# Kernel tuning notes

Hardware: AMD Instinct MI355X
Metric: run time of the kernel (lower is better)

Reference implementation:

```python
import jax, jax.numpy as jnp
import numpy as np

K_SIZE = 7
D_MODEL = 128
D_Q = 64
N_HEADS = 4
D_FF = 512
EPS = 1e-5


def _windows(x, k):
    # x: [N,E,H,W] -> [N,E,P,H,W]; zero-padded local k x k windows,
    # row-major over (dy,dx), matching nn.Unfold ordering.
    p = k // 2
    N, E, H, W = x.shape
    xp = jnp.pad(x, ((0, 0), (0, 0), (p, p), (p, p)))
    ws = [xp[:, :, i:i + H, j:j + W] for i in range(k) for j in range(k)]
    return jnp.stack(ws, axis=2)


def _layernorm(x, g, b):
    m = jnp.mean(x, -1, keepdims=True)
    v = jnp.var(x, -1, keepdims=True)
    return (x - m) * jax.lax.rsqrt(v + EPS) * g + b


def setup_inputs() -> dict:
    key = jax.random.key(0)
    ks = jax.random.split(key, 12)
    E, Q, F = D_MODEL, D_Q, D_FF

    def g(k, shape, s=0.02):
        return jax.random.normal(k, shape, jnp.float32) * s

    return dict(
        x=jax.random.normal(ks[0], (4, E, 64, 64), jnp.float32),
        qcoeff=jax.random.normal(ks[1], (4, Q), jnp.float32),
        wq=g(ks[2], (E, E)), bq=jnp.zeros((E,), jnp.float32),
        wk=g(ks[3], (E, E)), bk=jnp.zeros((E,), jnp.float32),
        wv=g(ks[4], (E, E)), bv=jnp.zeros((E,), jnp.float32),
        rel_bias=jnp.zeros((N_HEADS, K_SIZE * K_SIZE), jnp.float32),
        ln1_g=jnp.ones((E,), jnp.float32), ln1_b=jnp.zeros((E,), jnp.float32),
        bil_w=g(ks[5], (E, E, Q)), bil_b=jnp.zeros((E,), jnp.float32),
        ln2_g=jnp.ones((E,), jnp.float32), ln2_b=jnp.zeros((E,), jnp.float32),
        w1=g(ks[6], (F, E)), b1=jnp.zeros((F,), jnp.float32),
        w2=g(ks[7], (E, F)), b2=jnp.zeros((E,), jnp.float32),
    )


def reference(x, qcoeff, wq, bq, wk, bk, wv, bv, rel_bias, ln1_g, ln1_b,
              bil_w, bil_b, ln2_g, ln2_b, w1, b1, w2, b2):
    N, E, H, W = x.shape
    Nh = N_HEADS
    Hd = E // Nh
    P = K_SIZE * K_SIZE

    x_nhwc = jnp.transpose(x, (0, 2, 3, 1))              # [N,H,W,E]
    xn = _layernorm(x_nhwc, ln1_g, ln1_b)
    xnc = jnp.transpose(xn, (0, 3, 1, 2))                # [N,E,H,W]

    # 1x1-conv projections
    q = jnp.einsum('nchw,oc->nohw', xnc, wq) + bq[None, :, None, None]
    k = jnp.einsum('nchw,oc->nohw', xnc, wk) + bk[None, :, None, None]
    v = jnp.einsum('nchw,oc->nohw', xnc, wv) + bv[None, :, None, None]

    # local windows of K/V: [N,Nh,Hd,P,H,W]
    Kw = _windows(k, K_SIZE).reshape(N, Nh, Hd, P, H, W)
    Vw = _windows(v, K_SIZE).reshape(N, Nh, Hd, P, H, W)
    Qh = q.reshape(N, Nh, Hd, H, W)

    scores = jnp.einsum('nhdyx,nhdpyx->nhpyx', Qh, Kw)
    scores = scores + rel_bias[None, :, :, None, None]
    attn = jax.nn.softmax(scores, axis=2)                # softmax over P
    out = jnp.einsum('nhpyx,nhdpyx->nhdyx', attn, Vw).reshape(N, E, H, W)
    z0 = jnp.transpose(out, (0, 2, 3, 1))                # [N,H,W,E]

    # Bilinear(z0, qcoeff): qcoeff constant per (H,W) -> contract once per batch
    t = jnp.einsum('oiq,nq->noi', bil_w, qcoeff)         # [N,E,E]
    z1 = jnp.einsum('nhwi,noi->nhwo', z0, t) + bil_b

    z2 = z1 + x_nhwc
    z3 = _layernorm(z2, ln2_g, ln2_b)
    h1 = jax.nn.gelu(z3 @ w1.T + b1, approximate=False)  # dropout inactive (eval)
    z4 = h1 @ w2.T + b2 + z2
    return jnp.transpose(z4, (0, 3, 1, 2))               # [N,E,H,W]
```

## Files before the change

### kernel.cpp

```cpp
#include <hip/hip_runtime.h>
#include <cmath>

#define EPS 1e-5f
#define SZ 2097152

typedef __attribute__((ext_vector_type(8))) short short8;
typedef __attribute__((ext_vector_type(4))) float floatx4;

__device__ __forceinline__ float dot4(float4 a, float4 b) {
  return fmaf(a.x, b.x, fmaf(a.y, b.y, fmaf(a.z, b.z, a.w * b.w)));
}

__device__ __forceinline__ short f2bf(float f) {
  union { float f; unsigned u; } v; v.f = f;
  unsigned r = v.u + 0x7fff + ((v.u >> 16) & 1);
  return (short)(r >> 16);
}

#define MFMA16(a, b, c) __builtin_amdgcn_mfma_f32_16x16x32_bf16(a, b, c, 0, 0, 0)

__global__ __launch_bounds__(256) void k_prep(const float* __restrict__ w1,
    const float* __restrict__ w2, const float* __restrict__ wq,
    const float* __restrict__ wk, const float* __restrict__ wv,
    const float* __restrict__ bil_w, const float* __restrict__ qcoeff,
    short* __restrict__ w1bf, short* __restrict__ w2bf,
    short* __restrict__ wqbf, short* __restrict__ wkbf, short* __restrict__ wvbf,
    short* __restrict__ tb) {
  __shared__ float qs[256];
  int tid = threadIdx.x;
  qs[tid] = qcoeff[tid];
  __syncthreads();
  int tid0 = blockIdx.x * 256 + tid;
  int stride = gridDim.x * 256;
  for (int i = tid0; i < 16384; i += stride) {
    int flat = i * 4; int f = flat >> 7, c = flat & 127;
    float4 v = *(const float4*)&w1[flat];
    short t4[4] = {f2bf(v.x), f2bf(v.y), f2bf(v.z), f2bf(v.w)};
    *(uint2*)&w1bf[f * 136 + c] = *(uint2*)t4;
  }
  for (int i = tid0; i < 16384; i += stride) {
    int flat = i * 4; int o = flat >> 9, j = flat & 511;
    int ck = j >> 7, jj = j & 127;
    float4 v = *(const float4*)&w2[flat];
    short t4[4] = {f2bf(v.x), f2bf(v.y), f2bf(v.z), f2bf(v.w)};
    *(uint2*)&w2bf[(ck * 128 + o) * 136 + jj] = *(uint2*)t4;
  }
  for (int i = tid0; i < 4096; i += stride) {
    int flat = i * 4; int o = flat >> 7, c = flat & 127;
    float4 a = *(const float4*)&wq[flat];
    float4 b = *(const float4*)&wk[flat];
    float4 cc = *(const float4*)&wv[flat];
    short ta[4] = {f2bf(a.x), f2bf(a.y), f2bf(a.z), f2bf(a.w)};
    short tb4[4] = {f2bf(b.x), f2bf(b.y), f2bf(b.z), f2bf(b.w)};
    short tc[4] = {f2bf(cc.x), f2bf(cc.y), f2bf(cc.z), f2bf(cc.w)};
    *(uint2*)&wqbf[o * 136 + c] = *(uint2*)ta;
    *(uint2*)&wkbf[o * 136 + c] = *(uint2*)tb4;
    *(uint2*)&wvbf[o * 136 + c] = *(uint2*)tc;
  }
  {
    int flat = tid0;
    const float* wrow = bil_w + (size_t)flat * 64;
    float acc[4] = {0.f, 0.f, 0.f, 0.f};
    for (int qq = 0; qq < 64; qq += 4) {
      float4 w4 = *(const float4*)&wrow[qq];
#pragma unroll
      for (int nn = 0; nn < 4; ++nn) {
        const float* qc = &qs[nn * 64 + qq];
        acc[nn] = fmaf(w4.x, qc[0], fmaf(w4.y, qc[1], fmaf(w4.z, qc[2], fmaf(w4.w, qc[3], acc[nn]))));
      }
    }
    int o = flat >> 7, i = flat & 127;
#pragma unroll
    for (int nn = 0; nn < 4; ++nn) tb[nn * 17408 + o * 136 + i] = f2bf(acc[nn]);
  }
}

__global__ __launch_bounds__(1024) void k_qkvln(const float* __restrict__ x,
    const float* __restrict__ g, const float* __restrict__ b,
    const short* __restrict__ wqbf, const short* __restrict__ wkbf,
    const short* __restrict__ wvbf, const float* __restrict__ bq,
    const float* __restrict__ bk, const float* __restrict__ bv,
    float* __restrict__ xnhwc, short* __restrict__ qbf,
    short* __restrict__ kbf, short* __restrict__ vtb) {
  __shared__ float tile[128 * 65];
  __shared__ float mres[64], rres[64];
  __shared__ __align__(16) short xs[64 * 136];
  __shared__ __align__(16) short ws[128 * 136];
  int tid = threadIdx.x;
  int bid = blockIdx.x;
  int n = bid >> 6, y = bid & 63;
  const float* xb = x + (size_t)n * (128 * 4096) + y * 64;
  for (int it = 0; it < 8; ++it) {
    int flat = it * 1024 + tid;
    int c = flat >> 6, xp = flat & 63;
    tile[c * 65 + xp] = xb[(size_t)c * 4096 + xp];
  }
  __syncthreads();
  {
    int px = tid >> 4, cl = tid & 15;
    float s = 0.f, sq = 0.f;
#pragma unroll
    for (int j = 0; j < 8; ++j) {
      float v = tile[(cl * 8 + j) * 65 + px];
      s += v; sq += v * v;
    }
    s += __shfl_xor(s, 1);  sq += __shfl_xor(sq, 1);
    s += __shfl_xor(s, 2);  sq += __shfl_xor(sq, 2);
    s += __shfl_xor(s, 4);  sq += __shfl_xor(sq, 4);
    s += __shfl_xor(s, 8);  sq += __shfl_xor(sq, 8);
    if (cl == 0) {
      float m = s * (1.f / 128.f);
      float var = sq * (1.f / 128.f) - m * m;
      mres[px] = m;
      rres[px] = rsqrtf(var + EPS);
    }
  }
  __syncthreads();
  size_t rowbase = (size_t)bid * 8192;
  for (int it = 0; it < 8; ++it) {
    int flat = it * 1024 + tid;
    int c = flat & 127, px = flat >> 7;
    float v = tile[c * 65 + px];
    xnhwc[rowbase + flat] = v;
    xs[px * 136 + c] = f2bf((v - mres[px]) * rres[px] * g[c] + b[c]);
  }
  __syncthreads();
  int w = tid >> 6, lane = tid & 63;
  int quad = lane >> 4, r16 = lane & 15;
  int wm = w & 3, wn = w >> 2;
  int strip = wm * 16;
  short8 a[4];
#pragma unroll
  for (int kk = 0; kk < 4; ++kk)
    a[kk] = *(const short8*)&xs[(strip + r16) * 136 + kk * 32 + quad * 8];
  const short* wptr[3] = {wqbf, wkbf, wvbf};
  const float* bptr[3] = {bq, bk, bv};
  for (int m = 0; m < 3; ++m) {
    __syncthreads();
    const short* wp = wptr[m];
    for (int i = tid; i < 2176; i += 1024)
      *(short8*)&ws[i * 8] = *(const short8*)&wp[i * 8];
    __syncthreads();
    const float* bb = bptr[m];
#pragma unroll
    for (int nt = 0; nt < 2; ++nt) {
      int o0 = wn * 32 + nt * 16;
      floatx4 acc = {0.f, 0.f, 0.f, 0.f};
#pragma unroll
      for (int kk = 0; kk < 4; ++kk) {
        short8 bfr = *(const short8*)&ws[(o0 + r16) * 136 + kk * 32 + quad * 8];
        acc = MFMA16(a[kk], bfr, acc);
      }
      float bv2 = bb[o0 + r16];
      if (m < 2) {
        short* dst = (m == 0) ? qbf : kbf;
#pragma unroll
        for (int r = 0; r < 4; ++r) {
          int px = strip + quad * 4 + r;
          dst[rowbase + px * 128 + o0 + r16] = f2bf(acc[r] + bv2);
        }
      } else {
        short t4[4] = {f2bf(acc[0] + bv2), f2bf(acc[1] + bv2),
                       f2bf(acc[2] + bv2), f2bf(acc[3] + bv2)};
        *(uint2*)&vtb[(size_t)(n * 128 + o0 + r16) * 4096 + y * 64 + strip + quad * 4] =
            *(uint2*)t4;
      }
    }
  }
}

__global__ __launch_bounds__(256) void k_attn(const short* __restrict__ qbf,
    const short* __restrict__ kbf, const short* __restrict__ vtb,
    const float* __restrict__ rel_bias, float* __restrict__ z0) {
  __shared__ float ssf[4][16 * 50];
  __shared__ __align__(16) short AbB[4][16 * 68];
  __shared__ float biasS[4][52];
  int bid = blockIdx.x;
  int h = bid & 3, y = (bid >> 2) & 63, n = bid >> 8;
  int tid = threadIdx.x;
  int w = tid >> 6, lane = tid & 63;
  int quad = lane >> 4, r16 = lane & 15;
  int strip = w * 16;
  float* ssfw = ssf[w];
  short* Abw = AbB[w];
  float* biasw = biasS[w];
  {
    unsigned* ad = (unsigned*)Abw;
    for (int i = lane; i < 544; i += 64) ad[i] = 0u;
  }
  if (lane < 49) biasw[lane] = rel_bias[h * 49 + lane];
  const short* qrow = qbf + (size_t)n * 524288 + (size_t)y * 64 * 128 + h * 32;
  short8 qf = *(const short8*)&qrow[(strip + r16) * 128 + quad * 8];
  const short* kbp = kbf + (size_t)n * 524288 + h * 32;
#pragma unroll
  for (int r = 0; r < 7; ++r) {
    int yy = y + r - 3;
    bool yok = (unsigned)yy < 64u;
    int yyc = min(max(yy, 0), 63);
#pragma unroll
    for (int t = 0; t < 2; ++t) {
      int xxc = (w + t) * 16 + r16;
      int gx = xxc - 3;
      bool ok = yok && ((unsigned)gx < 64u);
      int gxc = min(max(gx, 0), 63);
      short8 bf = *(const short8*)&kbp[(size_t)(yyc * 64 + gxc) * 128 + quad * 8];
      floatx4 c = MFMA16(qf, bf, ((floatx4){0.f, 0.f, 0.f, 0.f}));
#pragma unroll
      for (int rr = 0; rr < 4; ++rr) {
        int lrow = quad * 4 + rr;
        int dx = xxc - (strip + lrow);
        if ((unsigned)dx < 7u) {
          float val = ok ? c[rr] : 0.f;
          ssfw[lrow * 50 + r * 7 + dx] = val + biasw[r * 7 + dx];
        }
      }
    }
  }
  {
    int lrow = lane >> 2, sub = lane & 3;
    int p0 = sub * 12, cnt = (sub == 3) ? 13 : 12;
    float sv[13];
    float mx = -1e30f;
    for (int pi = 0; pi < cnt; ++pi) { sv[pi] = ssfw[lrow * 50 + p0 + pi]; mx = fmaxf(mx, sv[pi]); }
    mx = fmaxf(mx, __shfl_xor(mx, 1));
    mx = fmaxf(mx, __shfl_xor(mx, 2));
    float sum = 0.f;
    for (int pi = 0; pi < cnt; ++pi) { float e = __expf(sv[pi] - mx); sv[pi] = e; sum += e; }
    sum += __shfl_xor(sum, 1);
    sum += __shfl_xor(sum, 2);
    float inv = 1.f / sum;
    for (int pi = 0; pi < cnt; ++pi) ssfw[lrow * 50 + p0 + pi] = sv[pi] * inv;
  }
  floatx4 oacc[2] = {(floatx4){0.f, 0.f, 0.f, 0.f}, (floatx4){0.f, 0.f, 0.f, 0.f}};
  int kk0 = (w == 3) ? 1 : 0;
  int kk1 = (w == 0) ? 0 : 1;
  int lrow = lane >> 2, sub = lane & 3;
  int pxg = strip + lrow;
  const short* vbp = vtb + (size_t)(n * 128 + h * 32) * 4096;
  for (int r = 0; r < 7; ++r) {
    int yy = y + r - 3;
    bool yok = (unsigned)yy < 64u;
    int yyc = min(max(yy, 0), 63);
    int c0 = pxg + sub - 3;
    if ((unsigned)c0 < 64u) Abw[lrow * 68 + c0] = f2bf(ssfw[lrow * 50 + r * 7 + sub]);
    int c1 = pxg + sub + 1;
    if (sub < 3 && (unsigned)c1 < 64u)
      Abw[lrow * 68 + c1] = f2bf(ssfw[lrow * 50 + r * 7 + sub + 4]);
    for (int kk = kk0; kk <= kk1; ++kk) {
      short8 af = *(const short8*)&Abw[r16 * 68 + kk * 32 + quad * 8];
#pragma unroll
      for (int nt = 0; nt < 2; ++nt) {
        short8 vf = *(const short8*)&vbp[(size_t)(nt * 16 + r16) * 4096 + yyc * 64 + kk * 32 + quad * 8];
        if (!yok) vf = (short8){0, 0, 0, 0, 0, 0, 0, 0};
        oacc[nt] = MFMA16(af, vf, oacc[nt]);
      }
    }
  }
  float* zrow = z0 + (size_t)n * 524288 + (size_t)y * 64 * 128 + h * 32;
#pragma unroll
  for (int nt = 0; nt < 2; ++nt)
#pragma unroll
    for (int rr = 0; rr < 4; ++rr) {
      int px = strip + quad * 4 + rr;
      zrow[px * 128 + nt * 16 + r16] = oacc[nt][rr];
    }
}

__global__ __launch_bounds__(1024) void k_tail(const float* __restrict__ z0,
    const short* __restrict__ tb, const float* __restrict__ bil_b,
    const float* __restrict__ xnhwc, const float* __restrict__ g2,
    const float* __restrict__ b2ln, const short* __restrict__ w1bf,
    const float* __restrict__ b1, const short* __restrict__ w2bf,
    const float* __restrict__ b2, float* __restrict__ out) {
  __shared__ __align__(16) char smem[34816 + 34816 + 17408 + 17408 + 33792];
  short* R1s = (short*)smem;
  short* w2c = (short*)(smem + 34816);
  short* z3s = (short*)(smem + 69632);
  short* h1s = (short*)(smem + 87040);
  float* z2s = (float*)(smem + 104448);
  float* outt = (float*)smem;
  int tid = threadIdx.x;
  int bid = blockIdx.x;
  int n = bid >> 6, y = bid & 63;
  size_t rowbase = (size_t)bid * 8192;
  for (int it = 0; it < 2; ++it) {
    int flat = (it * 1024 + tid) * 4;
    int px = flat >> 7, c = flat & 127;
    float4 v = *(const float4*)&z0[rowbase + flat];
    short tmp[4] = {f2bf(v.x), f2bf(v.y), f2bf(v.z), f2bf(v.w)};
    *(uint2*)&z3s[px * 136 + c] = *(uint2*)tmp;
  }
  const short* tn = tb + (size_t)n * 17408;
  for (int i = tid; i < 2176; i += 1024)
    *(short8*)&R1s[i * 8] = *(const short8*)&tn[i * 8];
  __syncthreads();
  int w = tid >> 6, lane = tid & 63;
  int quad = lane >> 4, r16 = lane & 15;
  int wm = w & 3, wn = w >> 2;
  int strip = wm * 16;
  {
    short8 a[4];
#pragma unroll
    for (int kk = 0; kk < 4; ++kk)
      a[kk] = *(const short8*)&z3s[(strip + r16) * 136 + kk * 32 + quad * 8];
#pragma unroll
    for (int nt = 0; nt < 2; ++nt) {
      int o0 = wn * 32 + nt * 16;
      floatx4 acc = {0.f, 0.f, 0.f, 0.f};
#pragma unroll
      for (int kk = 0; kk < 4; ++kk) {
        short8 bfr = *(const short8*)&R1s[(o0 + r16) * 136 + kk * 32 + quad * 8];
        acc = MFMA16(a[kk], bfr, acc);
      }
      float bb = bil_b[o0 + r16];
#pragma unroll
      for (int r = 0; r < 4; ++r) {
        int px = strip + quad * 4 + r;
        z2s[px * 132 + o0 + r16] = acc[r] + bb + xnhwc[rowbase + px * 128 + o0 + r16];
      }
    }
  }
  __syncthreads();
  {
    int px = tid >> 4, cl = tid & 15;
    float4 v0 = *(const float4*)&z2s[px * 132 + cl * 8];
    float4 v1 = *(const float4*)&z2s[px * 132 + cl * 8 + 4];
    float s = v0.x + v0.y + v0.z + v0.w + v1.x + v1.y + v1.z + v1.w;
    float sq = dot4(v0, v0) + dot4(v1, v1);
    s += __shfl_xor(s, 1);  sq += __shfl_xor(sq, 1);
    s += __shfl_xor(s, 2);  sq += __shfl_xor(sq, 2);
    s += __shfl_xor(s, 4);  sq += __shfl_xor(sq, 4);
    s += __shfl_xor(s, 8);  sq += __shfl_xor(sq, 8);
    float m = s * (1.f / 128.f);
    float var = sq * (1.f / 128.f) - m * m;
    float rr = rsqrtf(var + EPS);
    int c0 = cl * 8;
    short t8[8];
#pragma unroll
    for (int j = 0; j < 8; ++j) {
      float vv = (j < 4) ? (&v0.x)[j] : (&v1.x)[j - 4];
      t8[j] = f2bf((vv - m) * rr * g2[c0 + j] + b2ln[c0 + j]);
    }
    *(uint4*)&z3s[px * 136 + c0] = *(uint4*)t8;
  }
  __syncthreads();
  short8 a3[4];
#pragma unroll
  for (int kk = 0; kk < 4; ++kk)
    a3[kk] = *(const short8*)&z3s[(strip + r16) * 136 + kk * 32 + quad * 8];
  floatx4 zacc[2];
  zacc[0] = (floatx4){0.f, 0.f, 0.f, 0.f};
  zacc[1] = (floatx4){0.f, 0.f, 0.f, 0.f};
  for (int fc = 0; fc < 512; fc += 128) {
    __syncthreads();
    const short* w1src = w1bf + fc * 136;
    const short* w2src = w2bf + (fc >> 7) * 17408;
    for (int i = tid; i < 2176; i += 1024) {
      *(short8*)&R1s[i * 8] = *(const short8*)&w1src[i * 8];
      *(short8*)&w2c[i * 8] = *(const short8*)&w2src[i * 8];
    }
    __syncthreads();
#pragma unroll
    for (int nt = 0; nt < 2; ++nt) {
      int f0 = wn * 32 + nt * 16;
      floatx4 acc = {0.f, 0.f, 0.f, 0.f};
#pragma unroll
      for (int kk = 0; kk < 4; ++kk) {
        short8 bfr = *(const short8*)&R1s[(f0 + r16) * 136 + kk * 32 + quad * 8];
        acc = MFMA16(a3[kk], bfr, acc);
      }
      float bb1 = b1[fc + f0 + r16];
#pragma unroll
      for (int r = 0; r < 4; ++r) {
        float hv = acc[r] + bb1;
        float ge = 0.5f * hv * (1.f + erff(hv * 0.70710678118f));
        h1s[(strip + quad * 4 + r) * 136 + f0 + r16] = f2bf(ge);
      }
    }
    __syncthreads();
    short8 ah[4];
#pragma unroll
    for (int kk = 0; kk < 4; ++kk)
      ah[kk] = *(const short8*)&h1s[(strip + r16) * 136 + kk * 32 + quad * 8];
#pragma unroll
    for (int nt = 0; nt < 2; ++nt) {
      int o0 = wn * 32 + nt * 16;
#pragma unroll
      for (int kk = 0; kk < 4; ++kk) {
        short8 bfr = *(const short8*)&w2c[(o0 + r16) * 136 + kk * 32 + quad * 8];
        zacc[nt] = MFMA16(ah[kk], bfr, zacc[nt]);
      }
    }
  }
  __syncthreads();
#pragma unroll
  for (int nt = 0; nt < 2; ++nt) {
    int o0 = wn * 32 + nt * 16;
    float bb = b2[o0 + r16];
#pragma unroll
    for (int r = 0; r < 4; ++r) {
      int px = strip + quad * 4 + r;
      outt[(o0 + r16) * 65 + px] = zacc[nt][r] + bb + z2s[px * 132 + o0 + r16];
    }
  }
  __syncthreads();
  for (int it = 0; it < 8; ++it) {
    int flat = it * 1024 + tid;
    int o = flat >> 6, px = flat & 63;
    out[(((size_t)(n * 128 + o)) * 64 + y) * 64 + px] = outt[o * 65 + px];
  }
}

extern "C" void kernel_launch(void* const* d_in, const int* in_sizes, int n_in,
                              void* d_out, int out_size, void* d_ws, size_t ws_size,
                              hipStream_t stream) {
  const float* x        = (const float*)d_in[0];
  const float* qcoeff   = (const float*)d_in[1];
  const float* wq       = (const float*)d_in[2];
  const float* bq       = (const float*)d_in[3];
  const float* wk       = (const float*)d_in[4];
  const float* bk       = (const float*)d_in[5];
  const float* wv       = (const float*)d_in[6];
  const float* bv       = (const float*)d_in[7];
  const float* rel_bias = (const float*)d_in[8];
  const float* ln1_g    = (const float*)d_in[9];
  const float* ln1_b    = (const float*)d_in[10];
  const float* bil_w    = (const float*)d_in[11];
  const float* bil_b    = (const float*)d_in[12];
  const float* ln2_g    = (const float*)d_in[13];
  const float* ln2_b    = (const float*)d_in[14];
  const float* w1       = (const float*)d_in[15];
  const float* b1       = (const float*)d_in[16];
  const float* w2       = (const float*)d_in[17];
  const float* b2       = (const float*)d_in[18];
  float* out = (float*)d_out;

  float* ws = (float*)d_ws;
  float* x_nhwc = ws;
  float* z0     = ws + 1 * SZ;
  short* qbf = (short*)(ws + 2 * SZ);
  short* kbf = qbf + SZ;
  short* vtb = kbf + SZ;
  short* bf     = (short*)(ws + 4 * SZ);
  short* tb     = bf;
  short* w1bf   = bf + 4 * 17408;
  short* w2bf   = w1bf + 512 * 136;
  short* wqbf   = w2bf + 4 * 17408;
  short* wkbf   = wqbf + 17408;
  short* wvbf   = wkbf + 17408;

  k_prep<<<64, 256, 0, stream>>>(w1, w2, wq, wk, wv, bil_w, qcoeff,
                                 w1bf, w2bf, wqbf, wkbf, wvbf, tb);
  k_qkvln<<<256, 1024, 0, stream>>>(x, ln1_g, ln1_b, wqbf, wkbf, wvbf,
                                    bq, bk, bv, x_nhwc, qbf, kbf, vtb);
  k_attn<<<1024, 256, 0, stream>>>(qbf, kbf, vtb, rel_bias, z0);
  k_tail<<<256, 1024, 0, stream>>>(z0, tb, bil_b, x_nhwc, ln2_g, ln2_b,
                                   w1bf, b1, w2bf, b2, out);
}
```

Measured before the change: 151.7 us.

## Split qkvln and tail kernels into half-row blocks reading weights from global

k_qkvln and k_tail now process 32 pixels per block with 512 threads, launching 512 blocks instead of 256, so more blocks can spread across the GPU's compute units. Weight tiles are no longer staged into LDS. MFMA B-fragments are loaded directly from global memory (relying on L2/L1 caching), which removes the staging loops and several barriers and cuts LDS usage sharply. The trade-off is more global and cache traffic for weight fragments, and each weight is now fetched by twice as many blocks.

```diff
diff --git a/kernel.cpp b/kernel.cpp
--- a/kernel.cpp
+++ b/kernel.cpp
@@ -75,33 +75,33 @@
   }
 }
 
-__global__ __launch_bounds__(1024) void k_qkvln(const float* __restrict__ x,
+__global__ __launch_bounds__(512) void k_qkvln(const float* __restrict__ x,
     const float* __restrict__ g, const float* __restrict__ b,
     const short* __restrict__ wqbf, const short* __restrict__ wkbf,
     const short* __restrict__ wvbf, const float* __restrict__ bq,
     const float* __restrict__ bk, const float* __restrict__ bv,
     float* __restrict__ xnhwc, short* __restrict__ qbf,
     short* __restrict__ kbf, short* __restrict__ vtb) {
-  __shared__ float tile[128 * 65];
-  __shared__ float mres[64], rres[64];
-  __shared__ __align__(16) short xs[64 * 136];
-  __shared__ __align__(16) short ws[128 * 136];
+  __shared__ float tile[128 * 33];
+  __shared__ float mres[32], rres[32];
+  __shared__ __align__(16) short xs[32 * 136];
   int tid = threadIdx.x;
   int bid = blockIdx.x;
-  int n = bid >> 6, y = bid & 63;
-  const float* xb = x + (size_t)n * (128 * 4096) + y * 64;
+  int half = bid & 1, ny = bid >> 1;
+  int n = ny >> 6, y = ny & 63;
+  const float* xb = x + (size_t)n * 524288 + y * 64 + half * 32;
   for (int it = 0; it < 8; ++it) {
-    int flat = it * 1024 + tid;
-    int c = flat >> 6, xp = flat & 63;
-    tile[c * 65 + xp] = xb[(size_t)c * 4096 + xp];
-  }
-  __syncthreads();
-  {
-    int px = tid >> 4, cl = tid & 15;
+    int flat = it * 512 + tid;
+    int c = flat >> 5, xpl = flat & 31;
+    tile[c * 33 + xpl] = xb[(size_t)c * 4096 + xpl];
+  }
+  __syncthreads();
+  {
+    int pxl = tid >> 4, cl = tid & 15;
     float s = 0.f, sq = 0.f;
 #pragma unroll
     for (int j = 0; j < 8; ++j) {
-      float v = tile[(cl * 8 + j) * 65 + px];
+      float v = tile[(cl * 8 + j) * 33 + pxl];
       s += v; sq += v * v;
     }
     s += __shfl_xor(s, 1);  sq += __shfl_xor(sq, 1);
@@ -111,36 +111,32 @@
     if (cl == 0) {
       float m = s * (1.f / 128.f);
       float var = sq * (1.f / 128.f) - m * m;
-      mres[px] = m;
-      rres[px] = rsqrtf(var + EPS);
-    }
-  }
-  __syncthreads();
-  size_t rowbase = (size_t)bid * 8192;
+      mres[pxl] = m;
+      rres[pxl] = rsqrtf(var + EPS);
+    }
+  }
+  __syncthreads();
+  size_t rowbase = (size_t)ny * 8192 + half * 4096;
   for (int it = 0; it < 8; ++it) {
-    int flat = it * 1024 + tid;
-    int c = flat & 127, px = flat >> 7;
-    float v = tile[c * 65 + px];
+    int flat = it * 512 + tid;
+    int c = flat & 127, pxl = flat >> 7;
+    float v = tile[c * 33 + pxl];
     xnhwc[rowbase + flat] = v;
-    xs[px * 136 + c] = f2bf((v - mres[px]) * rres[px] * g[c] + b[c]);
+    xs[pxl * 136 + c] = f2bf((v - mres[pxl]) * rres[pxl] * g[c] + b[c]);
   }
   __syncthreads();
   int w = tid >> 6, lane = tid & 63;
   int quad = lane >> 4, r16 = lane & 15;
-  int wm = w & 3, wn = w >> 2;
-  int strip = wm * 16;
+  int wm = w & 1, wn = w >> 1;
+  int stripl = wm * 16;
   short8 a[4];
 #pragma unroll
   for (int kk = 0; kk < 4; ++kk)
-    a[kk] = *(const short8*)&xs[(strip + r16) * 136 + kk * 32 + quad * 8];
+    a[kk] = *(const short8*)&xs[(stripl + r16) * 136 + kk * 32 + quad * 8];
   const short* wptr[3] = {wqbf, wkbf, wvbf};
   const float* bptr[3] = {bq, bk, bv};
   for (int m = 0; m < 3; ++m) {
-    __syncthreads();
     const short* wp = wptr[m];
-    for (int i = tid; i < 2176; i += 1024)
-      *(short8*)&ws[i * 8] = *(const short8*)&wp[i * 8];
-    __syncthreads();
     const float* bb = bptr[m];
 #pragma unroll
     for (int nt = 0; nt < 2; ++nt) {
@@ -148,7 +144,7 @@
       floatx4 acc = {0.f, 0.f, 0.f, 0.f};
 #pragma unroll
       for (int kk = 0; kk < 4; ++kk) {
-        short8 bfr = *(const short8*)&ws[(o0 + r16) * 136 + kk * 32 + quad * 8];
+        short8 bfr = *(const short8*)&wp[(o0 + r16) * 136 + kk * 32 + quad * 8];
         acc = MFMA16(a[kk], bfr, acc);
       }
       float bv2 = bb[o0 + r16];
@@ -156,14 +152,14 @@
         short* dst = (m == 0) ? qbf : kbf;
 #pragma unroll
         for (int r = 0; r < 4; ++r) {
-          int px = strip + quad * 4 + r;
-          dst[rowbase + px * 128 + o0 + r16] = f2bf(acc[r] + bv2);
+          int pxl = stripl + quad * 4 + r;
+          dst[rowbase + pxl * 128 + o0 + r16] = f2bf(acc[r] + bv2);
         }
       } else {
         short t4[4] = {f2bf(acc[0] + bv2), f2bf(acc[1] + bv2),
                        f2bf(acc[2] + bv2), f2bf(acc[3] + bv2)};
-        *(uint2*)&vtb[(size_t)(n * 128 + o0 + r16) * 4096 + y * 64 + strip + quad * 4] =
-            *(uint2*)t4;
+        *(uint2*)&vtb[(size_t)(n * 128 + o0 + r16) * 4096 + y * 64 + half * 32 +
+                      stripl + quad * 4] = *(uint2*)t4;
       }
     }
   }
@@ -266,65 +262,62 @@
     }
 }
 
-__global__ __launch_bounds__(1024) void k_tail(const float* __restrict__ z0,
+__global__ __launch_bounds__(512) void k_tail(const float* __restrict__ z0,
     const short* __restrict__ tb, const float* __restrict__ bil_b,
     const float* __restrict__ xnhwc, const float* __restrict__ g2,
     const float* __restrict__ b2ln, const short* __restrict__ w1bf,
     const float* __restrict__ b1, const short* __restrict__ w2bf,
     const float* __restrict__ b2, float* __restrict__ out) {
-  __shared__ __align__(16) char smem[34816 + 34816 + 17408 + 17408 + 33792];
-  short* R1s = (short*)smem;
-  short* w2c = (short*)(smem + 34816);
-  short* z3s = (short*)(smem + 69632);
-  short* h1s = (short*)(smem + 87040);
-  float* z2s = (float*)(smem + 104448);
+  __shared__ __align__(16) char smem[8704 + 8704 + 16896];
+  short* z3s = (short*)smem;
+  short* h1s = (short*)(smem + 8704);
+  float* z2s = (float*)(smem + 17408);
   float* outt = (float*)smem;
   int tid = threadIdx.x;
   int bid = blockIdx.x;
-  int n = bid >> 6, y = bid & 63;
-  size_t rowbase = (size_t)bid * 8192;
+  int half = bid & 1, ny = bid >> 1;
+  int n = ny >> 6, y = ny & 63;
+  size_t rowbase = (size_t)ny * 8192 + half * 4096;
   for (int it = 0; it < 2; ++it) {
-    int flat = (it * 1024 + tid) * 4;
-    int px = flat >> 7, c = flat & 127;
+    int flat = (it * 512 + tid) * 4;
+    int pxl = flat >> 7, c = flat & 127;
     float4 v = *(const float4*)&z0[rowbase + flat];
     short tmp[4] = {f2bf(v.x), f2bf(v.y), f2bf(v.z), f2bf(v.w)};
-    *(uint2*)&z3s[px * 136 + c] = *(uint2*)tmp;
-  }
-  const short* tn = tb + (size_t)n * 17408;
-  for (int i = tid; i < 2176; i += 1024)
-    *(short8*)&R1s[i * 8] = *(const short8*)&tn[i * 8];
+    *(uint2*)&z3s[pxl * 136 + c] = *(uint2*)tmp;
+  }
   __syncthreads();
   int w = tid >> 6, lane = tid & 63;
   int quad = lane >> 4, r16 = lane & 15;
-  int wm = w & 3, wn = w >> 2;
-  int strip = wm * 16;
-  {
+  int wm = w & 1, wn = w >> 1;
+  int stripl = wm * 16;
+  {
+    const short* tn = tb + (size_t)n * 17408;
     short8 a[4];
 #pragma unroll
     for (int kk = 0; kk < 4; ++kk)
-      a[kk] = *(const short8*)&z3s[(strip + r16) * 136 + kk * 32 + quad * 8];
+      a[kk] = *(const short8*)&z3s[(stripl + r16) * 136 + kk * 32 + quad * 8];
 #pragma unroll
     for (int nt = 0; nt < 2; ++nt) {
       int o0 = wn * 32 + nt * 16;
       floatx4 acc = {0.f, 0.f, 0.f, 0.f};
 #pragma unroll
       for (int kk = 0; kk < 4; ++kk) {
-        short8 bfr = *(const short8*)&R1s[(o0 + r16) * 136 + kk * 32 + quad * 8];
+        short8 bfr = *(const short8*)&tn[(o0 + r16) * 136 + kk * 32 + quad * 8];
         acc = MFMA16(a[kk], bfr, acc);
       }
       float bb = bil_b[o0 + r16];
 #pragma unroll
       for (int r = 0; r < 4; ++r) {
-        int px = strip + quad * 4 + r;
-        z2s[px * 132 + o0 + r16] = acc[r] + bb + xnhwc[rowbase + px * 128 + o0 + r16];
-      }
-    }
-  }
-  __syncthreads();
-  {
-    int px = tid >> 4, cl = tid & 15;
-    float4 v0 = *(const float4*)&z2s[px * 132 + cl * 8];
-    float4 v1 = *(const float4*)&z2s[px * 132 + cl * 8 + 4];
+        int pxl = stripl + quad * 4 + r;
+        z2s[pxl * 132 + o0 + r16] = acc[r] + bb + xnhwc[rowbase + pxl * 128 + o0 + r16];
+      }
+    }
+  }
+  __syncthreads();
+  {
+    int pxl = tid >> 4, cl = tid & 15;
+    float4 v0 = *(const float4*)&z2s[pxl * 132 + cl * 8];
+    float4 v1 = *(const float4*)&z2s[pxl * 132 + cl * 8 + 4];
     float s = v0.x + v0.y + v0.z + v0.w + v1.x + v1.y + v1.z + v1.w;
     float sq = dot4(v0, v0) + dot4(v1, v1);
     s += __shfl_xor(s, 1);  sq += __shfl_xor(sq, 1);
@@ -341,32 +334,24 @@
       float vv = (j < 4) ? (&v0.x)[j] : (&v1.x)[j - 4];
       t8[j] = f2bf((vv - m) * rr * g2[c0 + j] + b2ln[c0 + j]);
     }
-    *(uint4*)&z3s[px * 136 + c0] = *(uint4*)t8;
+    *(uint4*)&z3s[pxl * 136 + c0] = *(uint4*)t8;
   }
   __syncthreads();
   short8 a3[4];
 #pragma unroll
   for (int kk = 0; kk < 4; ++kk)
-    a3[kk] = *(const short8*)&z3s[(strip + r16) * 136 + kk * 32 + quad * 8];
+    a3[kk] = *(const short8*)&z3s[(stripl + r16) * 136 + kk * 32 + quad * 8];
   floatx4 zacc[2];
   zacc[0] = (floatx4){0.f, 0.f, 0.f, 0.f};
   zacc[1] = (floatx4){0.f, 0.f, 0.f, 0.f};
   for (int fc = 0; fc < 512; fc += 128) {
-    __syncthreads();
-    const short* w1src = w1bf + fc * 136;
-    const short* w2src = w2bf + (fc >> 7) * 17408;
-    for (int i = tid; i < 2176; i += 1024) {
-      *(short8*)&R1s[i * 8] = *(const short8*)&w1src[i * 8];
-      *(short8*)&w2c[i * 8] = *(const short8*)&w2src[i * 8];
-    }
-    __syncthreads();
 #pragma unroll
     for (int nt = 0; nt < 2; ++nt) {
       int f0 = wn * 32 + nt * 16;
       floatx4 acc = {0.f, 0.f, 0.f, 0.f};
 #pragma unroll
       for (int kk = 0; kk < 4; ++kk) {
-        short8 bfr = *(const short8*)&R1s[(f0 + r16) * 136 + kk * 32 + quad * 8];
+        short8 bfr = *(const short8*)&w1bf[(fc + f0 + r16) * 136 + kk * 32 + quad * 8];
         acc = MFMA16(a3[kk], bfr, acc);
       }
       float bb1 = b1[fc + f0 + r16];
@@ -374,40 +359,41 @@
       for (int r = 0; r < 4; ++r) {
         float hv = acc[r] + bb1;
         float ge = 0.5f * hv * (1.f + erff(hv * 0.70710678118f));
-        h1s[(strip + quad * 4 + r) * 136 + f0 + r16] = f2bf(ge);
+        h1s[(stripl + quad * 4 + r) * 136 + f0 + r16] = f2bf(ge);
       }
     }
     __syncthreads();
     short8 ah[4];
 #pragma unroll
     for (int kk = 0; kk < 4; ++kk)
-      ah[kk] = *(const short8*)&h1s[(strip + r16) * 136 + kk * 32 + quad * 8];
+      ah[kk] = *(const short8*)&h1s[(stripl + r16) * 136 + kk * 32 + quad * 8];
+    const short* w2ck = w2bf + (fc >> 7) * 17408;
 #pragma unroll
     for (int nt = 0; nt < 2; ++nt) {
       int o0 = wn * 32 + nt * 16;
 #pragma unroll
       for (int kk = 0; kk < 4; ++kk) {
-        short8 bfr = *(const short8*)&w2c[(o0 + r16) * 136 + kk * 32 + quad * 8];
+        short8 bfr = *(const short8*)&w2ck[(o0 + r16) * 136 + kk * 32 + quad * 8];
         zacc[nt] = MFMA16(ah[kk], bfr, zacc[nt]);
       }
     }
-  }
-  __syncthreads();
+    __syncthreads();
+  }
 #pragma unroll
   for (int nt = 0; nt < 2; ++nt) {
     int o0 = wn * 32 + nt * 16;
     float bb = b2[o0 + r16];
 #pragma unroll
     for (int r = 0; r < 4; ++r) {
-      int px = strip + quad * 4 + r;
-      outt[(o0 + r16) * 65 + px] = zacc[nt][r] + bb + z2s[px * 132 + o0 + r16];
+      int pxl = stripl + quad * 4 + r;
+      outt[(o0 + r16) * 33 + pxl] = zacc[nt][r] + bb + z2s[pxl * 132 + o0 + r16];
     }
   }
   __syncthreads();
   for (int it = 0; it < 8; ++it) {
-    int flat = it * 1024 + tid;
-    int o = flat >> 6, px = flat & 63;
-    out[(((size_t)(n * 128 + o)) * 64 + y) * 64 + px] = outt[o * 65 + px];
+    int flat = it * 512 + tid;
+    int o = flat >> 5, pxl = flat & 31;
+    out[(((size_t)(n * 128 + o)) * 64 + y) * 64 + half * 32 + pxl] = outt[o * 33 + pxl];
   }
 }
 
@@ -451,9 +437,9 @@
 
   k_prep<<<64, 256, 0, stream>>>(w1, w2, wq, wk, wv, bil_w, qcoeff,
                                  w1bf, w2bf, wqbf, wkbf, wvbf, tb);
-  k_qkvln<<<256, 1024, 0, stream>>>(x, ln1_g, ln1_b, wqbf, wkbf, wvbf,
-                                    bq, bk, bv, x_nhwc, qbf, kbf, vtb);
+  k_qkvln<<<512, 512, 0, stream>>>(x, ln1_g, ln1_b, wqbf, wkbf, wvbf,
+                                   bq, bk, bv, x_nhwc, qbf, kbf, vtb);
   k_attn<<<1024, 256, 0, stream>>>(qbf, kbf, vtb, rel_bias, z0);
-  k_tail<<<256, 1024, 0, stream>>>(z0, tb, bil_b, x_nhwc, ln2_g, ln2_b,
-                                   w1bf, b1, w2bf, b2, out);
-}
+  k_tail<<<512, 512, 0, stream>>>(z0, tb, bil_b, x_nhwc, ln2_g, ln2_b,
+                                  w1bf, b1, w2bf, b2, out);
+}
```

Result: slower. 160.1 us (+5.5%).

## Fuse local attention into tail kernel, keeping attention output in shared memory

Applied to the files above, without the earlier changes.

Merges the attention kernel into the tail MLP kernel. Each 1024-thread block now computes attention for all four heads of one image row and writes the bf16 result straight into shared memory instead of a global fp32 z0 buffer. This removes one launch and the z0 write and reread. In exchange, the grid shrinks from 1024 blocks of 256 threads to 256 blocks of 1024 threads. Shared memory use grows to about 140KB, which could lower occupancy and overlap.

```diff
diff --git a/kernel.cpp b/kernel.cpp
--- a/kernel.cpp
+++ b/kernel.cpp
@@ -169,134 +169,119 @@
   }
 }
 
-__global__ __launch_bounds__(256) void k_attn(const short* __restrict__ qbf,
+__global__ __launch_bounds__(1024) void k_at(const short* __restrict__ qbf,
     const short* __restrict__ kbf, const short* __restrict__ vtb,
-    const float* __restrict__ rel_bias, float* __restrict__ z0) {
-  __shared__ float ssf[4][16 * 50];
-  __shared__ __align__(16) short AbB[4][16 * 68];
-  __shared__ float biasS[4][52];
-  int bid = blockIdx.x;
-  int h = bid & 3, y = (bid >> 2) & 63, n = bid >> 8;
-  int tid = threadIdx.x;
-  int w = tid >> 6, lane = tid & 63;
-  int quad = lane >> 4, r16 = lane & 15;
-  int strip = w * 16;
-  float* ssfw = ssf[w];
-  short* Abw = AbB[w];
-  float* biasw = biasS[w];
-  {
-    unsigned* ad = (unsigned*)Abw;
-    for (int i = lane; i < 544; i += 64) ad[i] = 0u;
-  }
-  if (lane < 49) biasw[lane] = rel_bias[h * 49 + lane];
-  const short* qrow = qbf + (size_t)n * 524288 + (size_t)y * 64 * 128 + h * 32;
-  short8 qf = *(const short8*)&qrow[(strip + r16) * 128 + quad * 8];
-  const short* kbp = kbf + (size_t)n * 524288 + h * 32;
-#pragma unroll
-  for (int r = 0; r < 7; ++r) {
-    int yy = y + r - 3;
-    bool yok = (unsigned)yy < 64u;
-    int yyc = min(max(yy, 0), 63);
-#pragma unroll
-    for (int t = 0; t < 2; ++t) {
-      int xxc = (w + t) * 16 + r16;
-      int gx = xxc - 3;
-      bool ok = yok && ((unsigned)gx < 64u);
-      int gxc = min(max(gx, 0), 63);
-      short8 bf = *(const short8*)&kbp[(size_t)(yyc * 64 + gxc) * 128 + quad * 8];
-      floatx4 c = MFMA16(qf, bf, ((floatx4){0.f, 0.f, 0.f, 0.f}));
-#pragma unroll
-      for (int rr = 0; rr < 4; ++rr) {
-        int lrow = quad * 4 + rr;
-        int dx = xxc - (strip + lrow);
-        if ((unsigned)dx < 7u) {
-          float val = ok ? c[rr] : 0.f;
-          ssfw[lrow * 50 + r * 7 + dx] = val + biasw[r * 7 + dx];
-        }
-      }
-    }
-  }
-  {
-    int lrow = lane >> 2, sub = lane & 3;
-    int p0 = sub * 12, cnt = (sub == 3) ? 13 : 12;
-    float sv[13];
-    float mx = -1e30f;
-    for (int pi = 0; pi < cnt; ++pi) { sv[pi] = ssfw[lrow * 50 + p0 + pi]; mx = fmaxf(mx, sv[pi]); }
-    mx = fmaxf(mx, __shfl_xor(mx, 1));
-    mx = fmaxf(mx, __shfl_xor(mx, 2));
-    float sum = 0.f;
-    for (int pi = 0; pi < cnt; ++pi) { float e = __expf(sv[pi] - mx); sv[pi] = e; sum += e; }
-    sum += __shfl_xor(sum, 1);
-    sum += __shfl_xor(sum, 2);
-    float inv = 1.f / sum;
-    for (int pi = 0; pi < cnt; ++pi) ssfw[lrow * 50 + p0 + pi] = sv[pi] * inv;
-  }
-  floatx4 oacc[2] = {(floatx4){0.f, 0.f, 0.f, 0.f}, (floatx4){0.f, 0.f, 0.f, 0.f}};
-  int kk0 = (w == 3) ? 1 : 0;
-  int kk1 = (w == 0) ? 0 : 1;
-  int lrow = lane >> 2, sub = lane & 3;
-  int pxg = strip + lrow;
-  const short* vbp = vtb + (size_t)(n * 128 + h * 32) * 4096;
-  for (int r = 0; r < 7; ++r) {
-    int yy = y + r - 3;
-    bool yok = (unsigned)yy < 64u;
-    int yyc = min(max(yy, 0), 63);
-    int c0 = pxg + sub - 3;
-    if ((unsigned)c0 < 64u) Abw[lrow * 68 + c0] = f2bf(ssfw[lrow * 50 + r * 7 + sub]);
-    int c1 = pxg + sub + 1;
-    if (sub < 3 && (unsigned)c1 < 64u)
-      Abw[lrow * 68 + c1] = f2bf(ssfw[lrow * 50 + r * 7 + sub + 4]);
-    for (int kk = kk0; kk <= kk1; ++kk) {
-      short8 af = *(const short8*)&Abw[r16 * 68 + kk * 32 + quad * 8];
-#pragma unroll
-      for (int nt = 0; nt < 2; ++nt) {
-        short8 vf = *(const short8*)&vbp[(size_t)(nt * 16 + r16) * 4096 + yyc * 64 + kk * 32 + quad * 8];
-        if (!yok) vf = (short8){0, 0, 0, 0, 0, 0, 0, 0};
-        oacc[nt] = MFMA16(af, vf, oacc[nt]);
-      }
-    }
-  }
-  float* zrow = z0 + (size_t)n * 524288 + (size_t)y * 64 * 128 + h * 32;
-#pragma unroll
-  for (int nt = 0; nt < 2; ++nt)
-#pragma unroll
-    for (int rr = 0; rr < 4; ++rr) {
-      int px = strip + quad * 4 + rr;
-      zrow[px * 128 + nt * 16 + r16] = oacc[nt][rr];
-    }
-}
-
-__global__ __launch_bounds__(1024) void k_tail(const float* __restrict__ z0,
-    const short* __restrict__ tb, const float* __restrict__ bil_b,
-    const float* __restrict__ xnhwc, const float* __restrict__ g2,
-    const float* __restrict__ b2ln, const short* __restrict__ w1bf,
-    const float* __restrict__ b1, const short* __restrict__ w2bf,
-    const float* __restrict__ b2, float* __restrict__ out) {
-  __shared__ __align__(16) char smem[34816 + 34816 + 17408 + 17408 + 33792];
-  short* R1s = (short*)smem;
-  short* w2c = (short*)(smem + 34816);
-  short* z3s = (short*)(smem + 69632);
-  short* h1s = (short*)(smem + 87040);
-  float* z2s = (float*)(smem + 104448);
-  float* outt = (float*)smem;
+    const float* __restrict__ rel_bias, const short* __restrict__ tb,
+    const float* __restrict__ bil_b, const float* __restrict__ xnhwc,
+    const float* __restrict__ g2, const float* __restrict__ b2ln,
+    const short* __restrict__ w1bf, const float* __restrict__ b1,
+    const short* __restrict__ w2bf, const float* __restrict__ b2,
+    float* __restrict__ out) {
+  __shared__ __align__(16) char smem[140544];
+  short* z3s = (short*)(smem + 89344);
+  float* z2s = (float*)(smem + 106752);
   int tid = threadIdx.x;
   int bid = blockIdx.x;
   int n = bid >> 6, y = bid & 63;
+  int w16 = tid >> 6, lane = tid & 63;
+  int quad = lane >> 4, r16 = lane & 15;
+  {
+    int h = w16 >> 2, sw = w16 & 3;
+    int strip = sw * 16;
+    float* ssfw = (float*)(smem + w16 * 3200);
+    short* Abw = (short*)(smem + 51200 + w16 * 2176);
+    float* biasw = (float*)(smem + 86016 + w16 * 208);
+    {
+      unsigned* ad = (unsigned*)Abw;
+      for (int i = lane; i < 544; i += 64) ad[i] = 0u;
+    }
+    if (lane < 49) biasw[lane] = rel_bias[h * 49 + lane];
+    const short* qrow = qbf + (size_t)n * 524288 + (size_t)y * 8192 + h * 32;
+    short8 qf = *(const short8*)&qrow[(strip + r16) * 128 + quad * 8];
+    const short* kbp = kbf + (size_t)n * 524288 + h * 32;
+#pragma unroll
+    for (int r = 0; r < 7; ++r) {
+      int yy = y + r - 3;
+      bool yok = (unsigned)yy < 64u;
+      int yyc = min(max(yy, 0), 63);
+#pragma unroll
+      for (int t = 0; t < 2; ++t) {
+        int xxc = (sw + t) * 16 + r16;
+        int gx = xxc - 3;
+        bool ok = yok && ((unsigned)gx < 64u);
+        int gxc = min(max(gx, 0), 63);
+        short8 bf = *(const short8*)&kbp[(size_t)(yyc * 64 + gxc) * 128 + quad * 8];
+        floatx4 c = MFMA16(qf, bf, ((floatx4){0.f, 0.f, 0.f, 0.f}));
+#pragma unroll
+        for (int rr = 0; rr < 4; ++rr) {
+          int lrow = quad * 4 + rr;
+          int dx = xxc - (strip + lrow);
+          if ((unsigned)dx < 7u) {
+            float val = ok ? c[rr] : 0.f;
+            ssfw[lrow * 50 + r * 7 + dx] = val + biasw[r * 7 + dx];
+          }
+        }
+      }
+    }
+    {
+      int lrow = lane >> 2, sub = lane & 3;
+      int p0 = sub * 12, cnt = (sub == 3) ? 13 : 12;
+      float sv[13];
+      float mx = -1e30f;
+      for (int pi = 0; pi < cnt; ++pi) { sv[pi] = ssfw[lrow * 50 + p0 + pi]; mx = fmaxf(mx, sv[pi]); }
+      mx = fmaxf(mx, __shfl_xor(mx, 1));
+      mx = fmaxf(mx, __shfl_xor(mx, 2));
+      float sum = 0.f;
+      for (int pi = 0; pi < cnt; ++pi) { float e = __expf(sv[pi] - mx); sv[pi] = e; sum += e; }
+      sum += __shfl_xor(sum, 1);
+      sum += __shfl_xor(sum, 2);
+      float inv = 1.f / sum;
+      for (int pi = 0; pi < cnt; ++pi) ssfw[lrow * 50 + p0 + pi] = sv[pi] * inv;
+    }
+    floatx4 oacc[2] = {(floatx4){0.f, 0.f, 0.f, 0.f}, (floatx4){0.f, 0.f, 0.f, 0.f}};
+    int kk0 = (sw == 3) ? 1 : 0;
+    int kk1 = (sw == 0) ? 0 : 1;
+    int lrow = lane >> 2, sub = lane & 3;
+    int pxg = strip + lrow;
+    const short* vbp = vtb + (size_t)(n * 128 + h * 32) * 4096;
+    for (int r = 0; r < 7; ++r) {
+      int yy = y + r - 3;
+      bool yok = (unsigned)yy < 64u;
+      int yyc = min(max(yy, 0), 63);
+      int c0 = pxg + sub - 3;
+      if ((unsigned)c0 < 64u) Abw[lrow * 68 + c0] = f2bf(ssfw[lrow * 50 + r * 7 + sub]);
+      int c1 = pxg + sub + 1;
+      if (sub < 3 && (unsigned)c1 < 64u)
+        Abw[lrow * 68 + c1] = f2bf(ssfw[lrow * 50 + r * 7 + sub + 4]);
+      for (int kk = kk0; kk <= kk1; ++kk) {
+        short8 af = *(const short8*)&Abw[r16 * 68 + kk * 32 + quad * 8];
+#pragma unroll
+        for (int nt = 0; nt < 2; ++nt) {
+          short8 vf = *(const short8*)&vbp[(size_t)(nt * 16 + r16) * 4096 + yyc * 64 + kk * 32 + quad * 8];
+          if (!yok) vf = (short8){0, 0, 0, 0, 0, 0, 0, 0};
+          oacc[nt] = MFMA16(af, vf, oacc[nt]);
+        }
+      }
+    }
+#pragma unroll
+    for (int nt = 0; nt < 2; ++nt)
+#pragma unroll
+      for (int rr = 0; rr < 4; ++rr) {
+        int px = strip + quad * 4 + rr;
+        z3s[px * 136 + h * 32 + nt * 16 + r16] = f2bf(oacc[nt][rr]);
+      }
+  }
+  __syncthreads();
+  short* R1s = (short*)smem;
+  short* w2c = (short*)(smem + 34816);
+  short* h1s = (short*)(smem + 69632);
+  float* outt = (float*)smem;
   size_t rowbase = (size_t)bid * 8192;
-  for (int it = 0; it < 2; ++it) {
-    int flat = (it * 1024 + tid) * 4;
-    int px = flat >> 7, c = flat & 127;
-    float4 v = *(const float4*)&z0[rowbase + flat];
-    short tmp[4] = {f2bf(v.x), f2bf(v.y), f2bf(v.z), f2bf(v.w)};
-    *(uint2*)&z3s[px * 136 + c] = *(uint2*)tmp;
-  }
   const short* tn = tb + (size_t)n * 17408;
   for (int i = tid; i < 2176; i += 1024)
     *(short8*)&R1s[i * 8] = *(const short8*)&tn[i * 8];
   __syncthreads();
-  int w = tid >> 6, lane = tid & 63;
-  int quad = lane >> 4, r16 = lane & 15;
-  int wm = w & 3, wn = w >> 2;
+  int wm = w16 & 3, wn = w16 >> 2;
   int strip = wm * 16;
   {
     short8 a[4];
@@ -437,7 +422,6 @@
 
   float* ws = (float*)d_ws;
   float* x_nhwc = ws;
-  float* z0     = ws + 1 * SZ;
   short* qbf = (short*)(ws + 2 * SZ);
   short* kbf = qbf + SZ;
   short* vtb = kbf + SZ;
@@ -453,7 +437,6 @@
                                  w1bf, w2bf, wqbf, wkbf, wvbf, tb);
   k_qkvln<<<256, 1024, 0, stream>>>(x, ln1_g, ln1_b, wqbf, wkbf, wvbf,
                                     bq, bk, bv, x_nhwc, qbf, kbf, vtb);
-  k_attn<<<1024, 256, 0, stream>>>(qbf, kbf, vtb, rel_bias, z0);
-  k_tail<<<256, 1024, 0, stream>>>(z0, tb, bil_b, x_nhwc, ln2_g, ln2_b,
-                                   w1bf, b1, w2bf, b2, out);
-}
+  k_at<<<256, 1024, 0, stream>>>(qbf, kbf, vtb, rel_bias, tb, bil_b, x_nhwc,
+                                 ln2_g, ln2_b, w1bf, b1, w2bf, b2, out);
+}
```

Measured after the change: 149.8 us. Within noise of the previous version (-1.2%).
